# Kernel optimization log

Measured on AMD Instinct MI355X. Metric: run time of the kernel, lower is better.

## Reference

```python
import jax, jax.numpy as jnp
import numpy as np

B, T, C = 2, 2048, 2048
H, KVH, HD = 16, 4, 128  # heads, kv heads, head_dim
G = H // KVH             # GQA group size
THETA = 10000.0


def _rope_cos_sin(t, hd, dtype):
    inv_freq = 1.0 / (THETA ** (jnp.arange(0, hd, 2, dtype=jnp.float32) / hd))
    pos = jnp.arange(t, dtype=jnp.float32)
    freqs = pos[:, None] * inv_freq[None, :]          # [T, hd/2]
    emb = jnp.concatenate([freqs, freqs], axis=-1)    # [T, hd]
    return jnp.cos(emb).astype(dtype), jnp.sin(emb).astype(dtype)


def _rotate_half(x):
    x1, x2 = jnp.split(x, 2, axis=-1)
    return jnp.concatenate([-x2, x1], axis=-1)


def setup_inputs() -> dict:
    key = jax.random.key(0)
    ks = jax.random.split(key, 5)
    s_in = 1.0 / np.sqrt(C)
    return {
        "x": jax.random.normal(ks[0], (B, T, C), jnp.float32),
        "wq": jax.random.normal(ks[1], (C, H * HD), jnp.float32) * s_in,
        "bq": jnp.zeros((H * HD,), jnp.float32),
        "wk": jax.random.normal(ks[2], (C, KVH * HD), jnp.float32) * s_in,
        "bk": jnp.zeros((KVH * HD,), jnp.float32),
        "wv": jax.random.normal(ks[3], (C, KVH * HD), jnp.float32) * s_in,
        "bv": jnp.zeros((KVH * HD,), jnp.float32),
        "wo": jax.random.normal(ks[4], (H * HD, C), jnp.float32) * (1.0 / np.sqrt(H * HD)),
    }


def reference(x, wq, bq, wk, bk, wv, bv, wo):
    b, t, c = x.shape
    q = (x @ wq + bq).reshape(b, t, H, HD).transpose(0, 2, 1, 3)    # [B,H,T,hd]
    k = (x @ wk + bk).reshape(b, t, KVH, HD).transpose(0, 2, 1, 3)  # [B,KVH,T,hd]
    v = (x @ wv + bv).reshape(b, t, KVH, HD).transpose(0, 2, 1, 3)

    cos, sin = _rope_cos_sin(t, HD, x.dtype)  # [T,hd]
    q = q * cos + _rotate_half(q) * sin
    k = k * cos + _rotate_half(k) * sin

    # GQA: group query heads over kv heads
    qg = q.reshape(b, KVH, G, t, HD)
    scale = 1.0 / np.sqrt(HD)
    scores = jnp.einsum('bkgtd,bksd->bkgts', qg, k) * scale  # [B,KVH,G,T,T]
    causal = jnp.tril(jnp.ones((t, t), bool))
    scores = jnp.where(causal, scores, jnp.finfo(scores.dtype).min)
    attn = jax.nn.softmax(scores, axis=-1)
    out = jnp.einsum('bkgts,bksd->bkgtd', attn, v)            # [B,KVH,G,T,hd]
    out = out.reshape(b, H, t, HD).transpose(0, 2, 1, 3).reshape(b, t, H * HD)
    return out @ wo
```

## Files before the change

kernel.cpp:

```cpp
#include <hip/hip_runtime.h>
#include <hip/hip_bf16.h>
#include <math.h>

#define B_ 2
#define T_ 2048
#define C_ 2048
#define H_ 16
#define KVH_ 4
#define HD_ 128
#define G_ (H_ / KVH_)
#define MROWS (B_ * T_)
#define NQKV (H_ * HD_ + 2 * KVH_ * HD_)
#define KOFF (H_ * HD_)
#define VOFF (H_ * HD_ + KVH_ * HD_)

typedef __hip_bfloat16 bf16;
typedef short bf16x8 __attribute__((ext_vector_type(8)));
typedef short bf16x4 __attribute__((ext_vector_type(4)));
typedef float f32x4 __attribute__((ext_vector_type(4)));

__device__ __forceinline__ void gload_lds16(const void* g, void* l) {
  __builtin_amdgcn_global_load_lds(
      (const __attribute__((address_space(1))) unsigned int*)g,
      (__attribute__((address_space(3))) unsigned int*)l, 16, 0, 0);
}

static __device__ __forceinline__ f32x4 mfma16(bf16x4 a, bf16x4 b, f32x4 c) {
#if __has_builtin(__builtin_amdgcn_mfma_f32_16x16x16_bf16)
  return __builtin_amdgcn_mfma_f32_16x16x16_bf16(a, b, c, 0, 0, 0);
#else
  return __builtin_amdgcn_mfma_f32_16x16x16bf16_1k(a, b, c, 0, 0, 0);
#endif
}

static __device__ __forceinline__ short f2bf(float x) {
  unsigned u = __builtin_bit_cast(unsigned, x);
  u += 0x7FFFu + ((u >> 16) & 1u);
  return (short)(u >> 16);
}

static __device__ __forceinline__ float fexp2(float x) {
#if __has_builtin(__builtin_amdgcn_exp2f)
  return __builtin_amdgcn_exp2f(x);
#else
  return exp2f(x);
#endif
}

__global__ void cast_bf16_kernel(const float* __restrict__ in, bf16* __restrict__ out, int n) {
  int i = (blockIdx.x * 256 + threadIdx.x) * 4;
  if (i >= n) return;
  float4 v = *(const float4*)(in + i);
  out[i + 0] = __float2bfloat16(v.x);
  out[i + 1] = __float2bfloat16(v.y);
  out[i + 2] = __float2bfloat16(v.z);
  out[i + 3] = __float2bfloat16(v.w);
}

__global__ __launch_bounds__(256) void transpose_cast(const float* __restrict__ in,
                                                      bf16* __restrict__ out,
                                                      int R, int Ccols) {
  __shared__ float t[32][33];
  const int tx = threadIdx.x & 31, ty = threadIdx.x >> 5;
  const int r0 = blockIdx.y * 32, c0 = blockIdx.x * 32;
#pragma unroll
  for (int it = 0; it < 4; ++it)
    t[ty + 8 * it][tx] = in[(size_t)(r0 + ty + 8 * it) * Ccols + c0 + tx];
  __syncthreads();
#pragma unroll
  for (int it = 0; it < 4; ++it)
    out[(size_t)(c0 + ty + 8 * it) * R + r0 + tx] = __float2bfloat16(t[tx][ty + 8 * it]);
}

__global__ __launch_bounds__(256) void transpose_cast_qkvw(
    const float* __restrict__ wq, const float* __restrict__ wk,
    const float* __restrict__ wv, bf16* __restrict__ outT) {
  __shared__ float t[32][33];
  const int tx = threadIdx.x & 31, ty = threadIdx.x >> 5;
  const int r0 = blockIdx.y * 32;
  const int c0 = blockIdx.x * 32;
  const float* src;
  int nn, ld;
  if (c0 < KOFF)      { src = wq; nn = c0;        ld = 2048; }
  else if (c0 < VOFF) { src = wk; nn = c0 - KOFF; ld = 512; }
  else                { src = wv; nn = c0 - VOFF; ld = 512; }
#pragma unroll
  for (int it = 0; it < 4; ++it)
    t[ty + 8 * it][tx] = src[(size_t)(r0 + ty + 8 * it) * ld + nn + tx];
  __syncthreads();
#pragma unroll
  for (int it = 0; it < 4; ++it)
    outT[(size_t)(c0 + ty + 8 * it) * 2048 + r0 + tx] = __float2bfloat16(t[tx][ty + 8 * it]);
}

__global__ __launch_bounds__(256) void transpose_v(const bf16* __restrict__ qkv,
                                                   bf16* __restrict__ vt) {
  __shared__ bf16 t[32][33];
  const int tx = threadIdx.x & 31, ty = threadIdx.x >> 5;
  const int b = blockIdx.z >> 2, kvh = blockIdx.z & 3;
  const int t0 = blockIdx.x * 32, d0 = blockIdx.y * 32;
#pragma unroll
  for (int it = 0; it < 4; ++it)
    t[ty + 8 * it][tx] =
        qkv[(size_t)(b * T_ + t0 + ty + 8 * it) * NQKV + VOFF + kvh * HD_ + d0 + tx];
  __syncthreads();
#pragma unroll
  for (int it = 0; it < 4; ++it)
    vt[((size_t)((b * KVH_ + kvh) * HD_) + d0 + ty + 8 * it) * T_ + t0 + tx] =
        t[tx][ty + 8 * it];
}

__global__ void rope_bf16(bf16* __restrict__ buf) {
  const int row = blockIdx.x / 20;
  const int hh = blockIdx.x % 20;
  const int t = row % T_;
  const int d = threadIdx.x;
  bf16* rp = buf + (size_t)row * NQKV + hh * HD_;
  float vd = __bfloat162float(rp[d]);
  float vp = __bfloat162float(rp[d ^ 64]);
  __syncthreads();
  const int i = d & 63;
  float invf = fexp2(-(float)i * (13.287712379549449f / 64.0f));
  float ang = (float)t * invf;
  float s, c;
  __sincosf(ang, &s, &c);
  rp[d] = __float2bfloat16((d < 64) ? (vd * c - vp * s) : (vd * c + vp * s));
}

template <bool BF16OUT>
__global__ __launch_bounds__(256, 2) void gemm_mfma(
    const bf16* __restrict__ A, const bf16* __restrict__ Bt, void* __restrict__ Cout,
    const float* __restrict__ bq, const float* __restrict__ bk2,
    const float* __restrict__ bv2, int M, int N, int K) {
  __shared__ __align__(16) bf16 As[128 * 32];
  __shared__ __align__(16) bf16 Bs[128 * 32];
  const int tid = threadIdx.x;
  const int w = tid >> 6, lane = tid & 63;
  const int colL = lane & 15, quad = lane >> 4;
  const int wm = w & 1, wn = w >> 1;
  const int r0 = blockIdx.y * 128, c0 = blockIdx.x * 128;

  f32x4 acc[4][4];
  const f32x4 zero = {0.f, 0.f, 0.f, 0.f};
#pragma unroll
  for (int mt = 0; mt < 4; ++mt)
#pragma unroll
    for (int nt = 0; nt < 4; ++nt) acc[mt][nt] = zero;

  for (int k0 = 0; k0 < K; k0 += 32) {
    __syncthreads();
#pragma unroll
    for (int it = 0; it < 2; ++it) {
      const int seg = it * 4 + w;
      const int idx = seg * 64 + lane;
      const int row = idx >> 2, off = idx & 3;
      gload_lds16(A + (size_t)(r0 + row) * K + k0 + off * 8, &As[seg * 512]);
      gload_lds16(Bt + (size_t)(c0 + row) * K + k0 + off * 8, &Bs[seg * 512]);
    }
    __syncthreads();
    bf16x8 af[4], bfv[4];
#pragma unroll
    for (int mt = 0; mt < 4; ++mt)
      af[mt] = *(const bf16x8*)&As[(wm * 64 + mt * 16 + colL) * 32 + quad * 8];
#pragma unroll
    for (int nt = 0; nt < 4; ++nt)
      bfv[nt] = *(const bf16x8*)&Bs[(wn * 64 + nt * 16 + colL) * 32 + quad * 8];
#pragma unroll
    for (int mt = 0; mt < 4; ++mt)
#pragma unroll
      for (int nt = 0; nt < 4; ++nt)
        acc[mt][nt] =
            __builtin_amdgcn_mfma_f32_16x16x32_bf16(af[mt], bfv[nt], acc[mt][nt], 0, 0, 0);
  }

#pragma unroll
  for (int nt = 0; nt < 4; ++nt) {
    const int c = c0 + wn * 64 + nt * 16 + colL;
    float bias = 0.f;
    if (bq) bias = (c < KOFF) ? bq[c] : (c < VOFF ? bk2[c - KOFF] : bv2[c - VOFF]);
#pragma unroll
    for (int mt = 0; mt < 4; ++mt) {
#pragma unroll
      for (int i = 0; i < 4; ++i) {
        const int r = r0 + wm * 64 + mt * 16 + quad * 4 + i;
        const float v = acc[mt][nt][i] + bias;
        if (BF16OUT)
          ((bf16*)Cout)[(size_t)r * N + c] = __float2bfloat16(v);
        else
          ((float*)Cout)[(size_t)r * N + c] = v;
      }
    }
  }
}

#define FA_SCL2 (0.08838834764831845f * 1.4426950408889634f)
#define FA_M2 16.0f

__global__ __launch_bounds__(128, 4) void flash_mfma6(
    const bf16* __restrict__ qkv, const bf16* __restrict__ vt, bf16* __restrict__ ao) {
  __shared__ __align__(16) char smem[49152];

  const int id = blockIdx.x;
  const int hb = id >> 4;
  const int qq = id & 15;
  const int h = hb & 15, b = hb >> 4;
  const int kvh = h >> 2;

  const int tid = threadIdx.x;
  const int w = tid >> 6, lane = tid & 63;
  const int colL = lane & 15, quad = lane >> 4;

  const bf16* kg = qkv + (size_t)(b * T_) * NQKV + KOFF + kvh * HD_;
  const bf16* vg = vt + (size_t)((b * KVH_ + kvh) * HD_) * T_;

  auto stageKV = [&](int tile, char* base) {
    bf16* kl = (bf16*)base;
    bf16* vl = (bf16*)(base + 8192);
    const int s0k = tile * 32;
#pragma unroll
    for (int j = 0; j < 4; ++j) {
      const int s = 4 * w + j;
      const int row = s * 4 + quad;
      const int g = colL ^ (row & 7);
      gload_lds16(kg + (size_t)(s0k + row) * NQKV + g * 8, kl + s * 512);
    }
#pragma unroll
    for (int j = 0; j < 4; ++j) {
      const int s = 4 * w + j;
      const int row = s * 16 + (lane >> 2);
      const int g = (lane & 3) ^ ((row >> 1) & 3);
      gload_lds16(vg + (size_t)row * T_ + s0k + g * 8, vl + s * 512);
    }
  };

#pragma unroll 1
  for (int pass = 0; pass < 2; ++pass) {
    const int qt = pass ? (31 - qq) : qq;
    const int myq0 = qt * 64 + 32 * w;
    const int nkv = 2 * qt + 2;

    bf16x8 qf[2][4];
    {
      const bf16* qgw = qkv + (size_t)(b * T_ + myq0) * NQKV + h * HD_;
#pragma unroll
      for (int mq = 0; mq < 2; ++mq)
#pragma unroll
        for (int c = 0; c < 4; ++c)
          qf[mq][c] = *(const bf16x8*)(qgw + (size_t)(mq * 16 + colL) * NQKV + c * 32 + quad * 8);
    }

    f32x4 o[2][8];
    const f32x4 zero = {0.f, 0.f, 0.f, 0.f};
#pragma unroll
    for (int mq = 0; mq < 2; ++mq)
#pragma unroll
      for (int ht = 0; ht < 8; ++ht) o[mq][ht] = zero;
    float l_[2] = {0.f, 0.f};

    stageKV(0, smem);
    stageKV(1, smem + 16384);
    asm volatile("s_waitcnt vmcnt(8)\n\ts_barrier" ::: "memory");

    int rb = 0, sb = 2;
#pragma unroll 1
    for (int tt = 0; tt < nkv; ++tt) {
      const bool pre = (tt + 2 < nkv);
      if (pre) stageKV(tt + 2, smem + sb * 16384);
      const bf16* Ks = (const bf16*)(smem + rb * 16384);
      const bf16* Vs = (const bf16*)(smem + rb * 16384 + 8192);

      const int s0 = tt * 32;
      if (s0 < myq0 + 32) {
        f32x4 s_[2][2];
        s_[0][0] = zero; s_[0][1] = zero; s_[1][0] = zero; s_[1][1] = zero;
#pragma unroll
        for (int c = 0; c < 4; ++c) {
          const int ch = ((c * 4 + quad) ^ (colL & 7)) * 8;
          bf16x8 kf0 = *(const bf16x8*)(Ks + (size_t)colL * 128 + ch);
          bf16x8 kf1 = *(const bf16x8*)(Ks + (size_t)(16 + colL) * 128 + ch);
#pragma unroll
          for (int mq = 0; mq < 2; ++mq) {
            s_[0][mq] = __builtin_amdgcn_mfma_f32_16x16x32_bf16(kf0, qf[mq][c], s_[0][mq], 0, 0, 0);
            s_[1][mq] = __builtin_amdgcn_mfma_f32_16x16x32_bf16(kf1, qf[mq][c], s_[1][mq], 0, 0, 0);
          }
        }

        bf16x4 pf[2][2];
        if (s0 >= myq0) {
#pragma unroll
          for (int kt = 0; kt < 2; ++kt)
#pragma unroll
            for (int mq = 0; mq < 2; ++mq) {
              const int qcol = myq0 + mq * 16 + colL;
              const int kb = s0 + kt * 16 + quad * 4;
              float pv[4];
#pragma unroll
              for (int i = 0; i < 4; ++i) {
                float e = fexp2(fmaf(s_[kt][mq][i], FA_SCL2, -FA_M2));
                pv[i] = (kb + i <= qcol) ? e : 0.f;
              }
              l_[mq] += (pv[0] + pv[1]) + (pv[2] + pv[3]);
              pf[kt][mq] = (bf16x4){f2bf(pv[0]), f2bf(pv[1]), f2bf(pv[2]), f2bf(pv[3])};
            }
        } else {
#pragma unroll
          for (int kt = 0; kt < 2; ++kt)
#pragma unroll
            for (int mq = 0; mq < 2; ++mq) {
              float pv[4];
#pragma unroll
              for (int i = 0; i < 4; ++i)
                pv[i] = fexp2(fmaf(s_[kt][mq][i], FA_SCL2, -FA_M2));
              l_[mq] += (pv[0] + pv[1]) + (pv[2] + pv[3]);
              pf[kt][mq] = (bf16x4){f2bf(pv[0]), f2bf(pv[1]), f2bf(pv[2]), f2bf(pv[3])};
            }
        }

#pragma unroll
        for (int ht = 0; ht < 8; ++ht) {
          const int row = ht * 16 + colL;
#pragma unroll
          for (int kt = 0; kt < 2; ++kt) {
            bf16x4 vf = *(const bf16x4*)(Vs + (size_t)row * 32 +
                                         (((kt * 2 + (quad >> 1)) ^ ((row >> 1) & 3)) * 8) +
                                         (quad & 1) * 4);
#pragma unroll
            for (int mq = 0; mq < 2; ++mq) o[mq][ht] = mfma16(vf, pf[kt][mq], o[mq][ht]);
          }
        }
      }

      if (pre)
        asm volatile("s_waitcnt vmcnt(8)\n\ts_barrier" ::: "memory");
      else
        asm volatile("s_waitcnt vmcnt(0)\n\ts_barrier" ::: "memory");
      rb = (rb == 2) ? 0 : rb + 1;
      sb = (sb == 2) ? 0 : sb + 1;
    }

#pragma unroll
    for (int mq = 0; mq < 2; ++mq) {
      float lv = l_[mq];
      lv += __shfl_xor(lv, 16);
      lv += __shfl_xor(lv, 32);
      const float rl = 1.f / lv;
      const size_t rbase = (size_t)(b * T_ + myq0 + mq * 16 + colL) * (H_ * HD_) + h * HD_;
#pragma unroll
      for (int ht = 0; ht < 8; ++ht) {
        bf16x4 ov;
#pragma unroll
        for (int i = 0; i < 4; ++i) ov[i] = f2bf(o[mq][ht][i] * rl);
        *(bf16x4*)(ao + rbase + ht * 16 + quad * 4) = ov;
      }
    }
  }
}

extern "C" void kernel_launch(void* const* d_in, const int* in_sizes, int n_in,
                              void* d_out, int out_size, void* d_ws, size_t ws_size,
                              hipStream_t stream) {
  (void)in_sizes; (void)n_in; (void)out_size; (void)ws_size;
  const float* x  = (const float*)d_in[0];
  const float* wq = (const float*)d_in[1];
  const float* bq = (const float*)d_in[2];
  const float* wk = (const float*)d_in[3];
  const float* bk = (const float*)d_in[4];
  const float* wv = (const float*)d_in[5];
  const float* bv = (const float*)d_in[6];
  const float* wo = (const float*)d_in[7];
  float* out = (float*)d_out;

  char* ws = (char*)d_ws;
  bf16* xb    = (bf16*)ws;
  bf16* wqkvT = (bf16*)(ws + (16u << 20));
  bf16* woT   = (bf16*)(ws + (28u << 20));
  bf16* qkv   = (bf16*)(ws + (36u << 20));
  bf16* vt    = (bf16*)(ws + (60u << 20));

  cast_bf16_kernel<<<dim3(MROWS * C_ / 1024), dim3(256), 0, stream>>>(x, xb, MROWS * C_);

  transpose_cast_qkvw<<<dim3(96, 64), dim3(256), 0, stream>>>(wq, wk, wv, wqkvT);
  transpose_cast<<<dim3(64, 64), dim3(256), 0, stream>>>(wo, woT, 2048, 2048);

  gemm_mfma<true><<<dim3(NQKV / 128, MROWS / 128), dim3(256), 0, stream>>>(
      xb, wqkvT, qkv, bq, bk, bv, MROWS, NQKV, C_);

  rope_bf16<<<dim3(MROWS * 20), dim3(128), 0, stream>>>(qkv);

  transpose_v<<<dim3(T_ / 32, HD_ / 32, B_ * KVH_), dim3(256), 0, stream>>>(qkv, vt);

  bf16* ao = xb;
  flash_mfma6<<<dim3(512), dim3(128), 0, stream>>>(qkv, vt, ao);

  gemm_mfma<false><<<dim3(C_ / 128, MROWS / 128), dim3(256), 0, stream>>>(
      ao, woT, out, nullptr, nullptr, nullptr, MROWS, C_, KOFF);
}
```

Before: 355.2 us.

## Pre-pack K/V into MFMA fragment layout and run single-wave LDS-free flash attention

Replaces the V transpose with two packing kernels that lay K and V tiles out in per-lane MFMA fragment order. The flash kernel becomes a one-wave block with 32 queries that loads K/V fragments straight from global memory into registers, with no LDS staging or barriers. It launches 2048 blocks, longest-first, instead of 512 blocks that each pair two query tiles. This removes LDS traffic and synchronisation, but adds a kernel launch, relies on L2/cache to serve K/V reused across the four query heads, and drops the explicit prefetch pipeline, so load latency is exposed.

```diff
diff --git a/kernel.cpp b/kernel.cpp
--- a/kernel.cpp
+++ b/kernel.cpp
@@ -91,23 +91,6 @@
 #pragma unroll
   for (int it = 0; it < 4; ++it)
     outT[(size_t)(c0 + ty + 8 * it) * 2048 + r0 + tx] = __float2bfloat16(t[tx][ty + 8 * it]);
-}
-
-__global__ __launch_bounds__(256) void transpose_v(const bf16* __restrict__ qkv,
-                                                   bf16* __restrict__ vt) {
-  __shared__ bf16 t[32][33];
-  const int tx = threadIdx.x & 31, ty = threadIdx.x >> 5;
-  const int b = blockIdx.z >> 2, kvh = blockIdx.z & 3;
-  const int t0 = blockIdx.x * 32, d0 = blockIdx.y * 32;
-#pragma unroll
-  for (int it = 0; it < 4; ++it)
-    t[ty + 8 * it][tx] =
-        qkv[(size_t)(b * T_ + t0 + ty + 8 * it) * NQKV + VOFF + kvh * HD_ + d0 + tx];
-  __syncthreads();
-#pragma unroll
-  for (int it = 0; it < 4; ++it)
-    vt[((size_t)((b * KVH_ + kvh) * HD_) + d0 + ty + 8 * it) * T_ + t0 + tx] =
-        t[tx][ty + 8 * it];
 }
 
 __global__ void rope_bf16(bf16* __restrict__ buf) {
@@ -127,6 +110,45 @@
   rp[d] = __float2bfloat16((d < 64) ? (vd * c - vp * s) : (vd * c + vp * s));
 }
 
+__global__ __launch_bounds__(256) void pack_k(const bf16* __restrict__ qkv,
+                                              bf16* __restrict__ kp) {
+  const int tile = blockIdx.x & 63;
+  const int bk = blockIdx.x >> 6;
+  const int b = bk >> 2, kvh = bk & 3;
+#pragma unroll
+  for (int u = 0; u < 2; ++u) {
+    const int t = threadIdx.x + u * 256;
+    const int kc = t >> 6, L = t & 63;
+    const bf16* src = qkv +
+        (size_t)(b * T_ + tile * 32 + 16 * (kc >> 2) + (L & 15)) * NQKV +
+        KOFF + kvh * HD_ + (kc & 3) * 32 + (L >> 4) * 8;
+    bf16x8 v = *(const bf16x8*)src;
+    *(bf16x8*)(kp + ((size_t)(bk * 64 + tile) * 8 + kc) * 512 + L * 8) = v;
+  }
+}
+
+__global__ __launch_bounds__(256) void pack_v(const bf16* __restrict__ qkv,
+                                              bf16* __restrict__ vp) {
+  const int tile = blockIdx.x & 63;
+  const int bk = blockIdx.x >> 6;
+  const int b = bk >> 2, kvh = bk & 3;
+#pragma unroll
+  for (int u = 0; u < 2; ++u) {
+    const int t = threadIdx.x + u * 256;
+    const int ht = t >> 6, L = t & 63;
+    const int colL = L & 15, quad = L >> 4;
+    const bf16* base = qkv + (size_t)(b * T_ + tile * 32 + quad * 4) * NQKV +
+                       VOFF + kvh * HD_ + ht * 16 + colL;
+    bf16x8 v;
+#pragma unroll
+    for (int j = 0; j < 4; ++j) {
+      v[j]     = *(const short*)(base + (size_t)j * NQKV);
+      v[j + 4] = *(const short*)(base + (size_t)(16 + j) * NQKV);
+    }
+    *(bf16x8*)(vp + ((size_t)(bk * 64 + tile) * 8 + ht) * 512 + L * 8) = v;
+  }
+}
+
 template <bool BF16OUT>
 __global__ __launch_bounds__(256, 2) void gemm_mfma(
     const bf16* __restrict__ A, const bf16* __restrict__ Bt, void* __restrict__ Cout,
@@ -196,162 +218,144 @@
 #define FA_SCL2 (0.08838834764831845f * 1.4426950408889634f)
 #define FA_M2 16.0f
 
-__global__ __launch_bounds__(128, 4) void flash_mfma6(
-    const bf16* __restrict__ qkv, const bf16* __restrict__ vt, bf16* __restrict__ ao) {
-  __shared__ __align__(16) char smem[49152];
-
+__global__ __launch_bounds__(64) void flash_mfma7(
+    const bf16* __restrict__ qkv, const bf16* __restrict__ kp,
+    const bf16* __restrict__ vp, bf16* __restrict__ ao) {
   const int id = blockIdx.x;
-  const int hb = id >> 4;
-  const int qq = id & 15;
+  const int j = 63 - (id & 63);
+  const int hb = id >> 6;
   const int h = hb & 15, b = hb >> 4;
-  const int kvh = h >> 2;
-
-  const int tid = threadIdx.x;
-  const int w = tid >> 6, lane = tid & 63;
+  const int bk = (b << 2) | (h >> 2);
+  const int lane = threadIdx.x & 63;
   const int colL = lane & 15, quad = lane >> 4;
-
-  const bf16* kg = qkv + (size_t)(b * T_) * NQKV + KOFF + kvh * HD_;
-  const bf16* vg = vt + (size_t)((b * KVH_ + kvh) * HD_) * T_;
-
-  auto stageKV = [&](int tile, char* base) {
-    bf16* kl = (bf16*)base;
-    bf16* vl = (bf16*)(base + 8192);
-    const int s0k = tile * 32;
-#pragma unroll
-    for (int j = 0; j < 4; ++j) {
-      const int s = 4 * w + j;
-      const int row = s * 4 + quad;
-      const int g = colL ^ (row & 7);
-      gload_lds16(kg + (size_t)(s0k + row) * NQKV + g * 8, kl + s * 512);
-    }
-#pragma unroll
-    for (int j = 0; j < 4; ++j) {
-      const int s = 4 * w + j;
-      const int row = s * 16 + (lane >> 2);
-      const int g = (lane & 3) ^ ((row >> 1) & 3);
-      gload_lds16(vg + (size_t)row * T_ + s0k + g * 8, vl + s * 512);
-    }
-  };
-
-#pragma unroll 1
-  for (int pass = 0; pass < 2; ++pass) {
-    const int qt = pass ? (31 - qq) : qq;
-    const int myq0 = qt * 64 + 32 * w;
-    const int nkv = 2 * qt + 2;
-
-    bf16x8 qf[2][4];
-    {
-      const bf16* qgw = qkv + (size_t)(b * T_ + myq0) * NQKV + h * HD_;
-#pragma unroll
-      for (int mq = 0; mq < 2; ++mq)
-#pragma unroll
-        for (int c = 0; c < 4; ++c)
-          qf[mq][c] = *(const bf16x8*)(qgw + (size_t)(mq * 16 + colL) * NQKV + c * 32 + quad * 8);
-    }
-
-    f32x4 o[2][8];
-    const f32x4 zero = {0.f, 0.f, 0.f, 0.f};
+  const int myq0 = j * 32;
+
+  bf16x8 qf[2][4];
+  {
+    const bf16* qg = qkv + (size_t)(b * T_ + myq0) * NQKV + h * HD_;
 #pragma unroll
     for (int mq = 0; mq < 2; ++mq)
 #pragma unroll
-      for (int ht = 0; ht < 8; ++ht) o[mq][ht] = zero;
-    float l_[2] = {0.f, 0.f};
-
-    stageKV(0, smem);
-    stageKV(1, smem + 16384);
-    asm volatile("s_waitcnt vmcnt(8)\n\ts_barrier" ::: "memory");
-
-    int rb = 0, sb = 2;
-#pragma unroll 1
-    for (int tt = 0; tt < nkv; ++tt) {
-      const bool pre = (tt + 2 < nkv);
-      if (pre) stageKV(tt + 2, smem + sb * 16384);
-      const bf16* Ks = (const bf16*)(smem + rb * 16384);
-      const bf16* Vs = (const bf16*)(smem + rb * 16384 + 8192);
-
-      const int s0 = tt * 32;
-      if (s0 < myq0 + 32) {
-        f32x4 s_[2][2];
-        s_[0][0] = zero; s_[0][1] = zero; s_[1][0] = zero; s_[1][1] = zero;
-#pragma unroll
-        for (int c = 0; c < 4; ++c) {
-          const int ch = ((c * 4 + quad) ^ (colL & 7)) * 8;
-          bf16x8 kf0 = *(const bf16x8*)(Ks + (size_t)colL * 128 + ch);
-          bf16x8 kf1 = *(const bf16x8*)(Ks + (size_t)(16 + colL) * 128 + ch);
-#pragma unroll
-          for (int mq = 0; mq < 2; ++mq) {
-            s_[0][mq] = __builtin_amdgcn_mfma_f32_16x16x32_bf16(kf0, qf[mq][c], s_[0][mq], 0, 0, 0);
-            s_[1][mq] = __builtin_amdgcn_mfma_f32_16x16x32_bf16(kf1, qf[mq][c], s_[1][mq], 0, 0, 0);
-          }
+      for (int c = 0; c < 4; ++c)
+        qf[mq][c] = *(const bf16x8*)(qg + (size_t)(mq * 16 + colL) * NQKV + c * 32 + quad * 8);
+  }
+
+  f32x4 o[2][8];
+  const f32x4 zero = {0.f, 0.f, 0.f, 0.f};
+#pragma unroll
+  for (int mq = 0; mq < 2; ++mq)
+#pragma unroll
+    for (int ht = 0; ht < 8; ++ht) o[mq][ht] = zero;
+  float l_[2] = {0.f, 0.f};
+
+  const bf16* kpb = kp + (size_t)bk * 64 * 4096 + lane * 8;
+  const bf16* vpb = vp + (size_t)bk * 64 * 4096 + lane * 8;
+
+  for (int tt = 0; tt < j; ++tt) {
+    const bf16* kt_ = kpb + (size_t)tt * 4096;
+    const bf16* vt_ = vpb + (size_t)tt * 4096;
+    bf16x8 kf[8], vf8[8];
+#pragma unroll
+    for (int kc = 0; kc < 8; ++kc) kf[kc] = *(const bf16x8*)(kt_ + kc * 512);
+#pragma unroll
+    for (int ht = 0; ht < 8; ++ht) vf8[ht] = *(const bf16x8*)(vt_ + ht * 512);
+
+    f32x4 s_[2][2];
+    s_[0][0] = zero; s_[0][1] = zero; s_[1][0] = zero; s_[1][1] = zero;
+#pragma unroll
+    for (int c = 0; c < 4; ++c)
+#pragma unroll
+      for (int mq = 0; mq < 2; ++mq) {
+        s_[0][mq] = __builtin_amdgcn_mfma_f32_16x16x32_bf16(kf[c],     qf[mq][c], s_[0][mq], 0, 0, 0);
+        s_[1][mq] = __builtin_amdgcn_mfma_f32_16x16x32_bf16(kf[4 + c], qf[mq][c], s_[1][mq], 0, 0, 0);
+      }
+
+    bf16x4 pf[2][2];
+#pragma unroll
+    for (int kt = 0; kt < 2; ++kt)
+#pragma unroll
+      for (int mq = 0; mq < 2; ++mq) {
+        float pv[4];
+#pragma unroll
+        for (int i = 0; i < 4; ++i)
+          pv[i] = fexp2(fmaf(s_[kt][mq][i], FA_SCL2, -FA_M2));
+        l_[mq] += (pv[0] + pv[1]) + (pv[2] + pv[3]);
+        pf[kt][mq] = (bf16x4){f2bf(pv[0]), f2bf(pv[1]), f2bf(pv[2]), f2bf(pv[3])};
+      }
+
+#pragma unroll
+    for (int ht = 0; ht < 8; ++ht) {
+      bf16x4 lo = __builtin_shufflevector(vf8[ht], vf8[ht], 0, 1, 2, 3);
+      bf16x4 hi = __builtin_shufflevector(vf8[ht], vf8[ht], 4, 5, 6, 7);
+#pragma unroll
+      for (int mq = 0; mq < 2; ++mq) {
+        o[mq][ht] = mfma16(lo, pf[0][mq], o[mq][ht]);
+        o[mq][ht] = mfma16(hi, pf[1][mq], o[mq][ht]);
+      }
+    }
+  }
+
+  {
+    const bf16* kt_ = kpb + (size_t)j * 4096;
+    const bf16* vt_ = vpb + (size_t)j * 4096;
+    bf16x8 kf[8], vf8[8];
+#pragma unroll
+    for (int kc = 0; kc < 8; ++kc) kf[kc] = *(const bf16x8*)(kt_ + kc * 512);
+#pragma unroll
+    for (int ht = 0; ht < 8; ++ht) vf8[ht] = *(const bf16x8*)(vt_ + ht * 512);
+
+    f32x4 s_[2][2];
+    s_[0][0] = zero; s_[0][1] = zero; s_[1][0] = zero; s_[1][1] = zero;
+#pragma unroll
+    for (int c = 0; c < 4; ++c)
+#pragma unroll
+      for (int mq = 0; mq < 2; ++mq) {
+        s_[0][mq] = __builtin_amdgcn_mfma_f32_16x16x32_bf16(kf[c],     qf[mq][c], s_[0][mq], 0, 0, 0);
+        s_[1][mq] = __builtin_amdgcn_mfma_f32_16x16x32_bf16(kf[4 + c], qf[mq][c], s_[1][mq], 0, 0, 0);
+      }
+
+    bf16x4 pf[2][2];
+#pragma unroll
+    for (int kt = 0; kt < 2; ++kt)
+#pragma unroll
+      for (int mq = 0; mq < 2; ++mq) {
+        const int qc = mq * 16 + colL;
+        const int kb = kt * 16 + quad * 4;
+        float pv[4];
+#pragma unroll
+        for (int i = 0; i < 4; ++i) {
+          float e = fexp2(fmaf(s_[kt][mq][i], FA_SCL2, -FA_M2));
+          pv[i] = (kb + i <= qc) ? e : 0.f;
         }
-
-        bf16x4 pf[2][2];
-        if (s0 >= myq0) {
-#pragma unroll
-          for (int kt = 0; kt < 2; ++kt)
-#pragma unroll
-            for (int mq = 0; mq < 2; ++mq) {
-              const int qcol = myq0 + mq * 16 + colL;
-              const int kb = s0 + kt * 16 + quad * 4;
-              float pv[4];
-#pragma unroll
-              for (int i = 0; i < 4; ++i) {
-                float e = fexp2(fmaf(s_[kt][mq][i], FA_SCL2, -FA_M2));
-                pv[i] = (kb + i <= qcol) ? e : 0.f;
-              }
-              l_[mq] += (pv[0] + pv[1]) + (pv[2] + pv[3]);
-              pf[kt][mq] = (bf16x4){f2bf(pv[0]), f2bf(pv[1]), f2bf(pv[2]), f2bf(pv[3])};
-            }
-        } else {
-#pragma unroll
-          for (int kt = 0; kt < 2; ++kt)
-#pragma unroll
-            for (int mq = 0; mq < 2; ++mq) {
-              float pv[4];
-#pragma unroll
-              for (int i = 0; i < 4; ++i)
-                pv[i] = fexp2(fmaf(s_[kt][mq][i], FA_SCL2, -FA_M2));
-              l_[mq] += (pv[0] + pv[1]) + (pv[2] + pv[3]);
-              pf[kt][mq] = (bf16x4){f2bf(pv[0]), f2bf(pv[1]), f2bf(pv[2]), f2bf(pv[3])};
-            }
-        }
-
-#pragma unroll
-        for (int ht = 0; ht < 8; ++ht) {
-          const int row = ht * 16 + colL;
-#pragma unroll
-          for (int kt = 0; kt < 2; ++kt) {
-            bf16x4 vf = *(const bf16x4*)(Vs + (size_t)row * 32 +
-                                         (((kt * 2 + (quad >> 1)) ^ ((row >> 1) & 3)) * 8) +
-                                         (quad & 1) * 4);
-#pragma unroll
-            for (int mq = 0; mq < 2; ++mq) o[mq][ht] = mfma16(vf, pf[kt][mq], o[mq][ht]);
-          }
-        }
-      }
-
-      if (pre)
-        asm volatile("s_waitcnt vmcnt(8)\n\ts_barrier" ::: "memory");
-      else
-        asm volatile("s_waitcnt vmcnt(0)\n\ts_barrier" ::: "memory");
-      rb = (rb == 2) ? 0 : rb + 1;
-      sb = (sb == 2) ? 0 : sb + 1;
-    }
-
-#pragma unroll
-    for (int mq = 0; mq < 2; ++mq) {
-      float lv = l_[mq];
-      lv += __shfl_xor(lv, 16);
-      lv += __shfl_xor(lv, 32);
-      const float rl = 1.f / lv;
-      const size_t rbase = (size_t)(b * T_ + myq0 + mq * 16 + colL) * (H_ * HD_) + h * HD_;
-#pragma unroll
-      for (int ht = 0; ht < 8; ++ht) {
-        bf16x4 ov;
-#pragma unroll
-        for (int i = 0; i < 4; ++i) ov[i] = f2bf(o[mq][ht][i] * rl);
-        *(bf16x4*)(ao + rbase + ht * 16 + quad * 4) = ov;
-      }
+        l_[mq] += (pv[0] + pv[1]) + (pv[2] + pv[3]);
+        pf[kt][mq] = (bf16x4){f2bf(pv[0]), f2bf(pv[1]), f2bf(pv[2]), f2bf(pv[3])};
+      }
+
+#pragma unroll
+    for (int ht = 0; ht < 8; ++ht) {
+      bf16x4 lo = __builtin_shufflevector(vf8[ht], vf8[ht], 0, 1, 2, 3);
+      bf16x4 hi = __builtin_shufflevector(vf8[ht], vf8[ht], 4, 5, 6, 7);
+#pragma unroll
+      for (int mq = 0; mq < 2; ++mq) {
+        o[mq][ht] = mfma16(lo, pf[0][mq], o[mq][ht]);
+        o[mq][ht] = mfma16(hi, pf[1][mq], o[mq][ht]);
+      }
+    }
+  }
+
+#pragma unroll
+  for (int mq = 0; mq < 2; ++mq) {
+    float lv = l_[mq];
+    lv += __shfl_xor(lv, 16);
+    lv += __shfl_xor(lv, 32);
+    const float rl = 1.f / lv;
+    const size_t rbase = (size_t)(b * T_ + myq0 + mq * 16 + colL) * (H_ * HD_) + h * HD_;
+#pragma unroll
+    for (int ht = 0; ht < 8; ++ht) {
+      bf16x4 ov;
+#pragma unroll
+      for (int i = 0; i < 4; ++i) ov[i] = f2bf(o[mq][ht][i] * rl);
+      *(bf16x4*)(ao + rbase + ht * 16 + quad * 4) = ov;
     }
   }
 }
@@ -375,7 +379,8 @@
   bf16* wqkvT = (bf16*)(ws + (16u << 20));
   bf16* woT   = (bf16*)(ws + (28u << 20));
   bf16* qkv   = (bf16*)(ws + (36u << 20));
-  bf16* vt    = (bf16*)(ws + (60u << 20));
+  bf16* kp    = (bf16*)(ws + (60u << 20));
+  bf16* vp    = (bf16*)(ws + (68u << 20));
 
   cast_bf16_kernel<<<dim3(MROWS * C_ / 1024), dim3(256), 0, stream>>>(x, xb, MROWS * C_);
 
@@ -387,10 +392,11 @@
 
   rope_bf16<<<dim3(MROWS * 20), dim3(128), 0, stream>>>(qkv);
 
-  transpose_v<<<dim3(T_ / 32, HD_ / 32, B_ * KVH_), dim3(256), 0, stream>>>(qkv, vt);
+  pack_k<<<dim3(8 * 64), dim3(256), 0, stream>>>(qkv, kp);
+  pack_v<<<dim3(8 * 64), dim3(256), 0, stream>>>(qkv, vp);
 
   bf16* ao = xb;
-  flash_mfma6<<<dim3(512), dim3(128), 0, stream>>>(qkv, vt, ao);
+  flash_mfma7<<<dim3(2048), dim3(64), 0, stream>>>(qkv, kp, vp, ao);
 
   gemm_mfma<false><<<dim3(C_ / 128, MROWS / 128), dim3(256), 0, stream>>>(
       ao, woT, out, nullptr, nullptr, nullptr, MROWS, C_, KOFF);
```

Measured after the change: 370.2 us. +4.2%, slower.
